# Kernel optimization log

Hardware: AMD Instinct MI355X
Metric: run time of the kernel (lower is better)

The kernel has to match this reference:

```python
import jax, jax.numpy as jnp
import numpy as np

B, H, W = 8, 512, 512          # batch, detector grid
M_PER_B = 32768
N = B * M_PER_B
C_IN, C_OUT, RED = 64, 128, 4
EPS = 1e-5


def setup_inputs() -> dict:
    key = jax.random.key(0)
    ks = jax.random.split(key, 8)
    # unique active-site indices per batch (permutation of flat grid cells)
    rng = np.random.default_rng(0)
    rows = []
    for b in range(B):
        flat = rng.permutation(H * W)[:M_PER_B]
        y, x = flat // W, flat % W
        rows.append(np.stack([np.full(M_PER_B, b), y, x], axis=1))
    indices = jnp.asarray(np.concatenate(rows, 0), dtype=jnp.int32)  # [N,3]

    feats = jax.random.normal(ks[0], (N, C_IN), jnp.float32)
    s1 = 1.0 / np.sqrt(9 * C_IN)
    s2 = 1.0 / np.sqrt(9 * C_OUT)
    return {
        "feats": feats,
        "indices": indices,
        "bn1_g": jnp.ones((C_IN,), jnp.float32),
        "bn1_b": jnp.zeros((C_IN,), jnp.float32),
        "w1": jax.random.normal(ks[1], (9, C_IN, C_OUT), jnp.float32) * s1,
        "bn2_g": jnp.ones((C_OUT,), jnp.float32),
        "bn2_b": jnp.zeros((C_OUT,), jnp.float32),
        "w2": jax.random.normal(ks[2], (9, C_OUT, C_OUT), jnp.float32) * s2,
        "fc1_w": jax.random.normal(ks[3], (C_OUT // RED, C_OUT), jnp.float32) / np.sqrt(C_OUT),
        "fc1_b": jnp.zeros((C_OUT // RED,), jnp.float32),
        "fc2_w": jax.random.normal(ks[4], (C_OUT, C_OUT // RED), jnp.float32) / np.sqrt(C_OUT // RED),
        "fc2_b": jnp.zeros((C_OUT,), jnp.float32),
        "w_skip": jax.random.normal(ks[5], (C_IN, C_OUT), jnp.float32) / np.sqrt(C_IN),
    }


def build_rulebook(indices):
    """Neighbor point-ids for each 3x3 offset. Returns ids [N,9], mask [N,9]."""
    n = indices.shape[0]
    b, y, x = indices[:, 0], indices[:, 1], indices[:, 2]
    grid = jnp.full((B, H, W), -1, jnp.int32).at[b, y, x].set(
        jnp.arange(n, dtype=jnp.int32))
    ids, masks = [], []
    for dy in (-1, 0, 1):
        for dx in (-1, 0, 1):
            ny, nx = y + dy, x + dx
            inb = (ny >= 0) & (ny < H) & (nx >= 0) & (nx < W)
            nid = grid[b, jnp.clip(ny, 0, H - 1), jnp.clip(nx, 0, W - 1)]
            m = inb & (nid >= 0)
            ids.append(jnp.where(m, nid, 0))
            masks.append(m)
    return jnp.stack(ids, 1), jnp.stack(masks, 1)


def subm_conv(f, nbr_ids, nbr_mask, w):
    """Submanifold 3x3 conv: gather-GEMM-scatter over active sites."""
    out = jnp.zeros((f.shape[0], w.shape[2]), f.dtype)
    for k in range(w.shape[0]):  # fixed 9 kernel offsets
        g = jnp.where(nbr_mask[:, k:k + 1], f[nbr_ids[:, k]], 0.0)
        out = out + g @ w[k]
    return out


def batchnorm(x, g, b):
    m = jnp.mean(x, 0)
    v = jnp.var(x, 0)  # biased, matches torch BN training normalization
    return (x - m) * jax.lax.rsqrt(v + EPS) * g + b


def reference(feats, indices, bn1_g, bn1_b, w1, bn2_g, bn2_b, w2,
              fc1_w, fc1_b, fc2_w, fc2_b, w_skip):
    nbr_ids, nbr_mask = build_rulebook(indices)  # shared indice_key rulebook
    bidx = indices[:, 0]

    out = jax.nn.relu(batchnorm(feats, bn1_g, bn1_b))
    out = subm_conv(out, nbr_ids, nbr_mask, w1)
    out = jax.nn.relu(batchnorm(out, bn2_g, bn2_b))
    out = subm_conv(out, nbr_ids, nbr_mask, w2)

    # SE: scatter-mean pool per event, FC-ReLU-FC-Sigmoid, per-site rescale
    pooled = jax.ops.segment_sum(out, bidx, num_segments=B)
    counts = jax.ops.segment_sum(jnp.ones((out.shape[0], 1), out.dtype), bidx,
                                 num_segments=B)
    pooled = pooled / jnp.clip(counts, 1.0, None)
    se = jax.nn.sigmoid(jax.nn.relu(pooled @ fc1_w.T + fc1_b) @ fc2_w.T + fc2_b)
    out = out * se[bidx]

    identity = feats @ w_skip  # 1x1 subm conv skip (in_ch != out_ch)
    return out + identity
```

## Files before the change

kernel.cpp:

```cpp
#include <hip/hip_runtime.h>
#include <math.h>

#define NPTS 262144
#define BB 8
#define HH 512
#define WW 512
#define EPSV 1e-5f

typedef short short8v __attribute__((ext_vector_type(8)));
typedef short short4v __attribute__((ext_vector_type(4)));
typedef float float4v __attribute__((ext_vector_type(4)));
typedef unsigned short ushort;
typedef ushort ushort8v __attribute__((ext_vector_type(8)));

static __device__ __forceinline__ ushort f2bf(float f) {
  union { float f; unsigned u; } v;
  v.f = f;
  unsigned r = v.u + 0x7fffu + ((v.u >> 16) & 1u);
  return (ushort)(r >> 16);
}

static __device__ __forceinline__ float bf2f(ushort h) {
  union { unsigned u; float f; } v;
  v.u = ((unsigned)h) << 16;
  return v.f;
}


__global__ __launch_bounds__(256) void k_scatter(const int* __restrict__ idx,
                                                 int* __restrict__ grid) {
  int i = blockIdx.x * 256 + threadIdx.x;
  int b = idx[i * 3 + 0], y = idx[i * 3 + 1], x = idx[i * 3 + 2];
  grid[(b * HH + y) * WW + x] = i;
}

__global__ __launch_bounds__(256) void k_rulebook(const int* __restrict__ idx,
                                                  const int* __restrict__ grid,
                                                  int* __restrict__ nbrT) {
  int i = blockIdx.x * 256 + threadIdx.x;
  int b = idx[i * 3 + 0], y = idx[i * 3 + 1], x = idx[i * 3 + 2];
  int t = 0;
  #pragma unroll
  for (int dy = -1; dy <= 1; ++dy) {
    #pragma unroll
    for (int dx = -1; dx <= 1; ++dx) {
      int ny = y + dy, nx = x + dx;
      int v = -1;
      if (ny >= 0 && ny < HH && nx >= 0 && nx < WW)
        v = grid[(b * HH + ny) * WW + nx];
      nbrT[(size_t)t * NPTS + i] = v;
      ++t;
    }
  }
}


__global__ __launch_bounds__(256) void k_stats64(const float* __restrict__ x,
                                                 float* __restrict__ sum,
                                                 float* __restrict__ ssum) {
  __shared__ float red_s[4][64];
  __shared__ float red_q[4][64];
  const int tid = threadIdx.x;
  const int lane = tid & 63;
  const int wave = tid >> 6;
  const int c4 = lane & 15;
  const int rq = lane >> 4;
  long long base = (long long)blockIdx.x * 256;
  float s0 = 0.f, s1 = 0.f, s2 = 0.f, s3 = 0.f;
  float q0 = 0.f, q1 = 0.f, q2 = 0.f, q3 = 0.f;
  for (int r = wave * 4 + rq; r < 256; r += 16) {
    float4 v = *(const float4*)(x + (base + r) * 64 + c4 * 4);
    s0 += v.x; s1 += v.y; s2 += v.z; s3 += v.w;
    q0 += v.x * v.x; q1 += v.y * v.y; q2 += v.z * v.z; q3 += v.w * v.w;
  }
  s0 += __shfl_xor(s0, 16, 64); s0 += __shfl_xor(s0, 32, 64);
  s1 += __shfl_xor(s1, 16, 64); s1 += __shfl_xor(s1, 32, 64);
  s2 += __shfl_xor(s2, 16, 64); s2 += __shfl_xor(s2, 32, 64);
  s3 += __shfl_xor(s3, 16, 64); s3 += __shfl_xor(s3, 32, 64);
  q0 += __shfl_xor(q0, 16, 64); q0 += __shfl_xor(q0, 32, 64);
  q1 += __shfl_xor(q1, 16, 64); q1 += __shfl_xor(q1, 32, 64);
  q2 += __shfl_xor(q2, 16, 64); q2 += __shfl_xor(q2, 32, 64);
  q3 += __shfl_xor(q3, 16, 64); q3 += __shfl_xor(q3, 32, 64);
  if (rq == 0) {
    red_s[wave][c4 * 4 + 0] = s0; red_s[wave][c4 * 4 + 1] = s1;
    red_s[wave][c4 * 4 + 2] = s2; red_s[wave][c4 * 4 + 3] = s3;
    red_q[wave][c4 * 4 + 0] = q0; red_q[wave][c4 * 4 + 1] = q1;
    red_q[wave][c4 * 4 + 2] = q2; red_q[wave][c4 * 4 + 3] = q3;
  }
  __syncthreads();
  if (tid < 64) {
    float ts = red_s[0][tid] + red_s[1][tid] + red_s[2][tid] + red_s[3][tid];
    float tq = red_q[0][tid] + red_q[1][tid] + red_q[2][tid] + red_q[3][tid];
    atomicAdd(&sum[tid], ts);
    atomicAdd(&ssum[tid], tq);
  }
}

template <int CI>
__global__ void k_finalize(const float* __restrict__ sum, const float* __restrict__ ssum,
                           const float* __restrict__ gam, const float* __restrict__ bet,
                           float* __restrict__ sc, float* __restrict__ sh) {
  int c = threadIdx.x;
  if (c < CI) {
    float m = sum[c] * (1.f / NPTS);
    float v = ssum[c] * (1.f / NPTS) - m * m;
    float s = gam[c] * rsqrtf(v + EPSV);
    sc[c] = s;
    sh[c] = bet[c] - m * s;
  }
}


__global__ __launch_bounds__(256) void k_norm1(const float* __restrict__ x,
                                               const float* __restrict__ sc,
                                               const float* __restrict__ sh,
                                               ushort* __restrict__ y) {
  long long i = ((long long)blockIdx.x * 256 + threadIdx.x) * 8;
  int c = (int)(i & 63);
  float4 a = *(const float4*)(x + i);
  float4 b = *(const float4*)(x + i + 4);
  float4 s0 = *(const float4*)(sc + c);
  float4 s1 = *(const float4*)(sc + c + 4);
  float4 h0 = *(const float4*)(sh + c);
  float4 h1 = *(const float4*)(sh + c + 4);
  ushort8v o;
  o[0] = f2bf(fmaxf(a.x * s0.x + h0.x, 0.f));
  o[1] = f2bf(fmaxf(a.y * s0.y + h0.y, 0.f));
  o[2] = f2bf(fmaxf(a.z * s0.z + h0.z, 0.f));
  o[3] = f2bf(fmaxf(a.w * s0.w + h0.w, 0.f));
  o[4] = f2bf(fmaxf(b.x * s1.x + h1.x, 0.f));
  o[5] = f2bf(fmaxf(b.y * s1.y + h1.y, 0.f));
  o[6] = f2bf(fmaxf(b.z * s1.z + h1.z, 0.f));
  o[7] = f2bf(fmaxf(b.w * s1.w + h1.w, 0.f));
  *(ushort8v*)(y + i) = o;
}

__global__ __launch_bounds__(256) void k_norm2(ushort* __restrict__ x,
                                               const float* __restrict__ sc,
                                               const float* __restrict__ sh) {
  long long i = ((long long)blockIdx.x * 256 + threadIdx.x) * 8;
  int c = (int)(i & 127);
  ushort8v v = *(const ushort8v*)(x + i);
  float4 s0 = *(const float4*)(sc + c);
  float4 s1 = *(const float4*)(sc + c + 4);
  float4 h0 = *(const float4*)(sh + c);
  float4 h1 = *(const float4*)(sh + c + 4);
  ushort8v o;
  o[0] = f2bf(fmaxf(bf2f(v[0]) * s0.x + h0.x, 0.f));
  o[1] = f2bf(fmaxf(bf2f(v[1]) * s0.y + h0.y, 0.f));
  o[2] = f2bf(fmaxf(bf2f(v[2]) * s0.z + h0.z, 0.f));
  o[3] = f2bf(fmaxf(bf2f(v[3]) * s0.w + h0.w, 0.f));
  o[4] = f2bf(fmaxf(bf2f(v[4]) * s1.x + h1.x, 0.f));
  o[5] = f2bf(fmaxf(bf2f(v[5]) * s1.y + h1.y, 0.f));
  o[6] = f2bf(fmaxf(bf2f(v[6]) * s1.z + h1.z, 0.f));
  o[7] = f2bf(fmaxf(bf2f(v[7]) * s1.w + h1.w, 0.f));
  *(ushort8v*)(x + i) = o;
}


__global__ __launch_bounds__(256) void k_wprep(const float* __restrict__ w,
                                               ushort* __restrict__ wt,
                                               int taps, int ci) {
  int i = blockIdx.x * 256 + threadIdx.x;
  int total = taps * ci * 128;
  if (i < total) {
    int t = i / (ci * 128);
    int rem = i - t * ci * 128;
    int c = rem >> 7;
    int o = rem & 127;
    wt[((size_t)t * 128 + o) * ci + c] = f2bf(w[i]);
  }
}


template <int CI, typename DstT, int EPI>
__global__ __launch_bounds__(256) void k_convd(const ushort* __restrict__ src,
                                               const int* __restrict__ nbrT,
                                               const ushort* __restrict__ wt,
                                               DstT* __restrict__ dst,
                                               float* __restrict__ e0,
                                               float* __restrict__ e1) {
  const int tid = threadIdx.x;
  const int base = blockIdx.x * 128;
  const int lane = tid & 63;
  const int wave = tid >> 6;
  const int wm = wave & 1, wn = wave >> 1;
  const int m_base = wm * 64, n_base = wn * 64;
  const int fm = lane & 15;
  const int fq = lane >> 4;
  const int koff = fq * 8;

  float4v acc[4][4];
  #pragma unroll
  for (int i = 0; i < 4; ++i)
    #pragma unroll
    for (int j = 0; j < 4; ++j) acc[i][j] = (float4v){0.f, 0.f, 0.f, 0.f};

  const int* nrow = nbrT + base + m_base + fm;

  for (int k = 0; k < 9; ++k) {
    int nid0 = nrow[(size_t)k * NPTS + 0];
    int nid1 = nrow[(size_t)k * NPTS + 16];
    int nid2 = nrow[(size_t)k * NPTS + 32];
    int nid3 = nrow[(size_t)k * NPTS + 48];
    const ushort* wrow = wt + ((size_t)k * 128 + n_base + fm) * CI + koff;
    #pragma unroll
    for (int kc = 0; kc < CI / 32; ++kc) {
      short8v bfr[4];
      #pragma unroll
      for (int ni = 0; ni < 4; ++ni)
        bfr[ni] = *(const short8v*)(wrow + ni * 16 * CI + kc * 32);
      const short8v z = {0, 0, 0, 0, 0, 0, 0, 0};
      short8v a0 = (nid0 >= 0) ? *(const short8v*)(src + (size_t)nid0 * CI + kc * 32 + koff) : z;
      short8v a1 = (nid1 >= 0) ? *(const short8v*)(src + (size_t)nid1 * CI + kc * 32 + koff) : z;
      short8v a2 = (nid2 >= 0) ? *(const short8v*)(src + (size_t)nid2 * CI + kc * 32 + koff) : z;
      short8v a3 = (nid3 >= 0) ? *(const short8v*)(src + (size_t)nid3 * CI + kc * 32 + koff) : z;
      #pragma unroll
      for (int ni = 0; ni < 4; ++ni) acc[0][ni] = __builtin_amdgcn_mfma_f32_16x16x32_bf16(a0, bfr[ni], acc[0][ni], 0, 0, 0);
      #pragma unroll
      for (int ni = 0; ni < 4; ++ni) acc[1][ni] = __builtin_amdgcn_mfma_f32_16x16x32_bf16(a1, bfr[ni], acc[1][ni], 0, 0, 0);
      #pragma unroll
      for (int ni = 0; ni < 4; ++ni) acc[2][ni] = __builtin_amdgcn_mfma_f32_16x16x32_bf16(a2, bfr[ni], acc[2][ni], 0, 0, 0);
      #pragma unroll
      for (int ni = 0; ni < 4; ++ni) acc[3][ni] = __builtin_amdgcn_mfma_f32_16x16x32_bf16(a3, bfr[ni], acc[3][ni], 0, 0, 0);
    }
  }

  float es[4], ess[4];
  if constexpr (EPI) {
    #pragma unroll
    for (int ni = 0; ni < 4; ++ni) { es[ni] = 0.f; ess[ni] = 0.f; }
  }
  #pragma unroll
  for (int mi = 0; mi < 4; ++mi) {
    #pragma unroll
    for (int ni = 0; ni < 4; ++ni) {
      int pt = base + m_base + mi * 16 + fq * 4;
      int co = n_base + ni * 16 + fm;
      float4v c = acc[mi][ni];
      #pragma unroll
      for (int r = 0; r < 4; ++r) {
        if constexpr (sizeof(DstT) == 4) {
          ((float*)dst)[(size_t)(pt + r) * 128 + co] = c[r];
          if constexpr (EPI == 2) es[ni] += c[r];
        } else {
          ushort h = f2bf(c[r]);
          ((ushort*)dst)[(size_t)(pt + r) * 128 + co] = h;
          if constexpr (EPI == 1) {
            float v = bf2f(h);
            es[ni] += v;
            ess[ni] += v * v;
          }
        }
      }
    }
  }

  if constexpr (EPI) {
    #pragma unroll
    for (int ni = 0; ni < 4; ++ni) {
      float s = es[ni];
      s += __shfl_xor(s, 16, 64);
      s += __shfl_xor(s, 32, 64);
      float q = 0.f;
      if constexpr (EPI == 1) {
        q = ess[ni];
        q += __shfl_xor(q, 16, 64);
        q += __shfl_xor(q, 32, 64);
      }
      if (fq == 0) {
        int co = n_base + ni * 16 + fm;
        if constexpr (EPI == 1) {
          atomicAdd(&e0[co], s);
          atomicAdd(&e1[co], q);
        } else {
          int b = base >> 15;
          atomicAdd(&e0[b * 128 + co], s);
        }
      }
    }
  }
}


template <typename SrcT, typename DstT, int CI, int TAPS, bool ACT, int EPI>
__global__ __launch_bounds__(256) void k_conv(const SrcT* __restrict__ src,
                                              const float* __restrict__ scale,
                                              const float* __restrict__ shift,
                                              const int* __restrict__ nbrT,
                                              const ushort* __restrict__ wt,
                                              DstT* __restrict__ dst,
                                              float* __restrict__ e0,
                                              float* __restrict__ e1) {
  constexpr int SA = CI + 8;
  __shared__ ushort As[128 * SA];
  __shared__ ushort Bs[128 * SA];
  __shared__ float s_sc[CI], s_sh[CI];

  const int tid = threadIdx.x;
  const int base = blockIdx.x * 128;
  const int lane = tid & 63;
  const int wave = tid >> 6;
  const int wm = wave & 1, wn = wave >> 1;
  const int m_base = wm * 64, n_base = wn * 64;
  const int fm = lane & 15;
  const int fq = lane >> 4;

  if constexpr (ACT) {
    for (int c = tid; c < CI; c += 256) {
      s_sc[c] = scale[c];
      s_sh[c] = shift[c];
    }
  }
  __syncthreads();

  float4v acc[4][4];
  #pragma unroll
  for (int i = 0; i < 4; ++i)
    #pragma unroll
    for (int j = 0; j < 4; ++j) acc[i][j] = (float4v){0.f, 0.f, 0.f, 0.f};

  const int srow_i = tid >> 1;
  const int shalf = tid & 1;
  const int c0 = shalf * (CI / 2);

  for (int k = 0; k < TAPS; ++k) {
    if (k) __syncthreads();

    int nid;
    if constexpr (TAPS == 1) {
      nid = base + srow_i;
    } else {
      nid = nbrT[(size_t)k * NPTS + base + srow_i];
    }
    ushort* arow = &As[srow_i * SA + c0];
    if (nid >= 0) {
      const SrcT* gsrc = src + (size_t)nid * CI + c0;
      if constexpr (sizeof(SrcT) == 4) {
        #pragma unroll
        for (int j = 0; j < CI / 2; j += 4) {
          float4 v = *(const float4*)((const float*)gsrc + j);
          if constexpr (ACT) {
            int c = c0 + j;
            v.x = fmaxf(v.x * s_sc[c + 0] + s_sh[c + 0], 0.f);
            v.y = fmaxf(v.y * s_sc[c + 1] + s_sh[c + 1], 0.f);
            v.z = fmaxf(v.z * s_sc[c + 2] + s_sh[c + 2], 0.f);
            v.w = fmaxf(v.w * s_sc[c + 3] + s_sh[c + 3], 0.f);
          }
          short4v o = {(short)f2bf(v.x), (short)f2bf(v.y), (short)f2bf(v.z), (short)f2bf(v.w)};
          *(short4v*)(arow + j) = o;
        }
      } else {
        #pragma unroll
        for (int j = 0; j < CI / 2; j += 8) {
          ushort8v raw = *(const ushort8v*)((const ushort*)gsrc + j);
          short8v o;
          #pragma unroll
          for (int e = 0; e < 8; ++e) {
            float f = bf2f(raw[e]);
            if constexpr (ACT) {
              int c = c0 + j + e;
              f = fmaxf(f * s_sc[c] + s_sh[c], 0.f);
            }
            o[e] = (short)f2bf(f);
          }
          *(short8v*)(arow + j) = o;
        }
      }
    } else {
      #pragma unroll
      for (int j = 0; j < CI / 2; j += 4)
        *(short4v*)(arow + j) = (short4v){0, 0, 0, 0};
    }

    {
      const ushort* wrow = wt + ((size_t)k * 128 + srow_i) * CI + c0;
      ushort* brow = &Bs[srow_i * SA + c0];
      #pragma unroll
      for (int j = 0; j < CI / 2; j += 8)
        *(uint4*)(brow + j) = *(const uint4*)(wrow + j);
    }
    __syncthreads();

    #pragma unroll
    for (int kc = 0; kc < CI / 32; ++kc) {
      short8v af[4], bf[4];
      #pragma unroll
      for (int mi = 0; mi < 4; ++mi)
        af[mi] = *(const short8v*)(&As[(m_base + mi * 16 + fm) * SA + kc * 32 + fq * 8]);
      #pragma unroll
      for (int ni = 0; ni < 4; ++ni)
        bf[ni] = *(const short8v*)(&Bs[(n_base + ni * 16 + fm) * SA + kc * 32 + fq * 8]);
      #pragma unroll
      for (int mi = 0; mi < 4; ++mi)
        #pragma unroll
        for (int ni = 0; ni < 4; ++ni)
          acc[mi][ni] = __builtin_amdgcn_mfma_f32_16x16x32_bf16(af[mi], bf[ni], acc[mi][ni], 0, 0, 0);
    }
  }

  float es[4], ess[4];
  if constexpr (EPI) {
    #pragma unroll
    for (int ni = 0; ni < 4; ++ni) { es[ni] = 0.f; ess[ni] = 0.f; }
  }
  #pragma unroll
  for (int mi = 0; mi < 4; ++mi) {
    #pragma unroll
    for (int ni = 0; ni < 4; ++ni) {
      int pt = base + m_base + mi * 16 + fq * 4;
      int co = n_base + ni * 16 + fm;
      float4v c = acc[mi][ni];
      #pragma unroll
      for (int r = 0; r < 4; ++r) {
        if constexpr (sizeof(DstT) == 4) {
          ((float*)dst)[(size_t)(pt + r) * 128 + co] = c[r];
          if constexpr (EPI == 2) es[ni] += c[r];
        } else {
          ushort h = f2bf(c[r]);
          ((ushort*)dst)[(size_t)(pt + r) * 128 + co] = h;
          if constexpr (EPI == 1) {
            float v = bf2f(h);
            es[ni] += v;
            ess[ni] += v * v;
          }
        }
      }
    }
  }

  if constexpr (EPI) {
    #pragma unroll
    for (int ni = 0; ni < 4; ++ni) {
      float s = es[ni];
      s += __shfl_xor(s, 16, 64);
      s += __shfl_xor(s, 32, 64);
      float q = 0.f;
      if constexpr (EPI == 1) {
        q = ess[ni];
        q += __shfl_xor(q, 16, 64);
        q += __shfl_xor(q, 32, 64);
      }
      if (fq == 0) {
        int co = n_base + ni * 16 + fm;
        if constexpr (EPI == 1) {
          atomicAdd(&e0[co], s);
          atomicAdd(&e1[co], q);
        } else {
          int b = base >> 15;
          atomicAdd(&e0[b * 128 + co], s);
        }
      }
    }
  }
}


__global__ __launch_bounds__(256) void k_se(const float* __restrict__ pooled,
                                            const float* __restrict__ fc1w,
                                            const float* __restrict__ fc1b,
                                            const float* __restrict__ fc2w,
                                            const float* __restrict__ fc2b,
                                            float* __restrict__ se) {
  __shared__ float h[8][32];
  int tid = threadIdx.x;
  int b = tid >> 5, j = tid & 31;
  float s = fc1b[j];
  for (int c = 0; c < 128; ++c)
    s += pooled[b * 128 + c] * (1.f / 32768.f) * fc1w[j * 128 + c];
  h[b][j] = fmaxf(s, 0.f);
  __syncthreads();
  for (int t = tid; t < 1024; t += 256) {
    int bb = t >> 7, c = t & 127;
    float s2 = fc2b[c];
    #pragma unroll
    for (int jj = 0; jj < 32; ++jj) s2 += h[bb][jj] * fc2w[c * 32 + jj];
    se[t] = 1.f / (1.f + expf(-s2));
  }
}

__global__ __launch_bounds__(256) void k_final(float* __restrict__ out,
                                               const ushort* __restrict__ id,
                                               const float* __restrict__ se) {
  long long i = ((long long)blockIdx.x * 256 + threadIdx.x) * 4;
  int co = (int)(i & 127);
  long long rowi = i >> 7;
  int b = (int)(rowi >> 15);
  float4 o = *(const float4*)(out + i);
  ushort dh[4];
  *(uint2*)dh = *(const uint2*)(id + i);
  float4 s = *(const float4*)(se + b * 128 + co);
  o.x = o.x * s.x + bf2f(dh[0]);
  o.y = o.y * s.y + bf2f(dh[1]);
  o.z = o.z * s.z + bf2f(dh[2]);
  o.w = o.w * s.w + bf2f(dh[3]);
  *(float4*)(out + i) = o;
}


extern "C" void kernel_launch(void* const* d_in, const int* in_sizes, int n_in,
                              void* d_out, int out_size, void* d_ws, size_t ws_size,
                              hipStream_t stream) {
  const float* feats = (const float*)d_in[0];
  const int* indices = (const int*)d_in[1];
  const float* bn1_g = (const float*)d_in[2];
  const float* bn1_b = (const float*)d_in[3];
  const float* w1    = (const float*)d_in[4];
  const float* bn2_g = (const float*)d_in[5];
  const float* bn2_b = (const float*)d_in[6];
  const float* w2    = (const float*)d_in[7];
  const float* fc1w  = (const float*)d_in[8];
  const float* fc1b  = (const float*)d_in[9];
  const float* fc2w  = (const float*)d_in[10];
  const float* fc2b  = (const float*)d_in[11];
  const float* wskip = (const float*)d_in[12];
  float* out = (float*)d_out;

  char* p = (char*)d_ws;
  int* nbrT = (int*)p;      p += (size_t)NPTS * 9 * 4;
  float* stats = (float*)p; p += 4096 * 4;
  ushort* wt1 = (ushort*)p; p += (size_t)9 * 128 * 64 * 2;
  ushort* wt2 = (ushort*)p; p += (size_t)9 * 128 * 128 * 2;
  ushort* wts = (ushort*)p; p += (size_t)128 * 64 * 2;
  p = (char*)(((size_t)p + 255) & ~(size_t)255);

  float* sum1 = stats, *ss1 = stats + 64, *sc1 = stats + 128, *sh1 = stats + 192;
  float* sum2 = stats + 256, *ss2 = stats + 384, *sc2 = stats + 512, *sh2 = stats + 640;
  float* pooled = stats + 768;
  float* se = stats + 1792;

  size_t fixed = (size_t)(p - (char*)d_ws);
  size_t need_new = fixed + (size_t)NPTS * 64 * 2 + (size_t)NPTS * 128 * 2;
  bool big = ws_size >= need_new;

  hipMemsetAsync(stats, 0, 4096 * 4, stream);

  if (big) {
    int* grid_i = (int*)p;
    ushort* featsn = (ushort*)p;
    ushort* out1 = (ushort*)(p + (size_t)NPTS * 64 * 2);

    hipMemsetAsync(grid_i, 0xFF, (size_t)BB * HH * WW * 4, stream);
    k_scatter<<<NPTS / 256, 256, 0, stream>>>(indices, grid_i);
    k_rulebook<<<NPTS / 256, 256, 0, stream>>>(indices, grid_i, nbrT);

    k_wprep<<<(9 * 64 * 128 + 255) / 256, 256, 0, stream>>>(w1, wt1, 9, 64);
    k_wprep<<<(9 * 128 * 128 + 255) / 256, 256, 0, stream>>>(w2, wt2, 9, 128);
    k_wprep<<<(64 * 128 + 255) / 256, 256, 0, stream>>>(wskip, wts, 1, 64);

    k_stats64<<<NPTS / 256, 256, 0, stream>>>(feats, sum1, ss1);
    k_finalize<64><<<1, 64, 0, stream>>>(sum1, ss1, bn1_g, bn1_b, sc1, sh1);

    k_norm1<<<NPTS * 64 / 8 / 256, 256, 0, stream>>>(feats, sc1, sh1, featsn);

    k_convd<64, ushort, 1><<<NPTS / 128, 256, 0, stream>>>(
        featsn, nbrT, wt1, out1, sum2, ss2);

    k_finalize<128><<<1, 128, 0, stream>>>(sum2, ss2, bn2_g, bn2_b, sc2, sh2);

    k_norm2<<<NPTS * 128 / 8 / 256, 256, 0, stream>>>(out1, sc2, sh2);

    k_convd<128, float, 2><<<NPTS / 128, 256, 0, stream>>>(
        out1, nbrT, wt2, out, pooled, nullptr);

    k_conv<float, ushort, 64, 1, false, 0><<<NPTS / 128, 256, 0, stream>>>(
        feats, nullptr, nullptr, nullptr, wts, out1, nullptr, nullptr);

    k_se<<<1, 256, 0, stream>>>(pooled, fc1w, fc1b, fc2w, fc2b, se);
    k_final<<<NPTS * 128 / 1024, 256, 0, stream>>>(out, out1, se);
  } else {
    int* grid_i = (int*)p;
    ushort* out1 = (ushort*)p;

    hipMemsetAsync(grid_i, 0xFF, (size_t)BB * HH * WW * 4, stream);
    k_scatter<<<NPTS / 256, 256, 0, stream>>>(indices, grid_i);
    k_rulebook<<<NPTS / 256, 256, 0, stream>>>(indices, grid_i, nbrT);

    k_wprep<<<(9 * 64 * 128 + 255) / 256, 256, 0, stream>>>(w1, wt1, 9, 64);
    k_wprep<<<(9 * 128 * 128 + 255) / 256, 256, 0, stream>>>(w2, wt2, 9, 128);
    k_wprep<<<(64 * 128 + 255) / 256, 256, 0, stream>>>(wskip, wts, 1, 64);

    k_stats64<<<NPTS / 256, 256, 0, stream>>>(feats, sum1, ss1);
    k_finalize<64><<<1, 64, 0, stream>>>(sum1, ss1, bn1_g, bn1_b, sc1, sh1);

    k_conv<float, ushort, 64, 9, true, 1><<<NPTS / 128, 256, 0, stream>>>(
        feats, sc1, sh1, nbrT, wt1, out1, sum2, ss2);

    k_finalize<128><<<1, 128, 0, stream>>>(sum2, ss2, bn2_g, bn2_b, sc2, sh2);

    k_conv<ushort, float, 128, 9, true, 2><<<NPTS / 128, 256, 0, stream>>>(
        out1, sc2, sh2, nbrT, wt2, out, pooled, nullptr);

    k_conv<float, ushort, 64, 1, false, 0><<<NPTS / 128, 256, 0, stream>>>(
        feats, nullptr, nullptr, nullptr, wts, out1, nullptr, nullptr);

    k_se<<<1, 256, 0, stream>>>(pooled, fc1w, fc1b, fc2w, fc2b, se);
    k_final<<<NPTS * 128 / 1024, 256, 0, stream>>>(out, out1, se);
  }
}
```

Measured before the change: 710.0 us.

## Stage gathered neighbor rows in swizzled LDS with register prefetch of next tap

The direct-gather conv kernel now gathers each tap's 128 neighbor feature rows cooperatively into XOR-swizzled shared memory. While MFMAs run on the current tap, it prefetches the next tap's gathered rows and the neighbor ids two taps ahead in registers. Previously each wave read the A fragments straight from global memory with 16-byte loads per lane. The block index is also remapped to interleave blocks across the point range. The change costs extra LDS, two barriers per tap, and more register pressure, which may reduce occupancy.

New measurement: 689.1 us. -2.9%, faster.

```diff
diff --git a/kernel.cpp b/kernel.cpp
--- a/kernel.cpp
+++ b/kernel.cpp
@@ -174,21 +174,31 @@
 
 
 template <int CI, typename DstT, int EPI>
-__global__ __launch_bounds__(256) void k_convd(const ushort* __restrict__ src,
+__global__ __launch_bounds__(256) void k_convp(const ushort* __restrict__ src,
                                                const int* __restrict__ nbrT,
                                                const ushort* __restrict__ wt,
                                                DstT* __restrict__ dst,
                                                float* __restrict__ e0,
                                                float* __restrict__ e1) {
+  constexpr int CHUNKS = CI / 8;
+  constexpr int RPI    = 64 / CHUNKS;
+  constexpr int NSTG   = 32 / RPI;
+  __shared__ ushort As[128 * CI];
+
   const int tid = threadIdx.x;
-  const int base = blockIdx.x * 128;
+  int bidx = blockIdx.x;
+  bidx = (bidx & 7) * ((NPTS / 128) / 8) + (bidx >> 3);
+  const int base = bidx * 128;
   const int lane = tid & 63;
   const int wave = tid >> 6;
   const int wm = wave & 1, wn = wave >> 1;
   const int m_base = wm * 64, n_base = wn * 64;
   const int fm = lane & 15;
   const int fq = lane >> 4;
-  const int koff = fq * 8;
+
+  const int s_rl = lane / CHUNKS;
+  const int s_c  = lane % CHUNKS;
+  const int srow0 = wave * 32 + s_rl;
 
   float4v acc[4][4];
   #pragma unroll
@@ -196,33 +206,74 @@
     #pragma unroll
     for (int j = 0; j < 4; ++j) acc[i][j] = (float4v){0.f, 0.f, 0.f, 0.f};
 
-  const int* nrow = nbrT + base + m_base + fm;
-
+  int nr[2][NSTG];
+  uint4 g[NSTG];
+
+  #pragma unroll
+  for (int i = 0; i < NSTG; ++i)
+    nr[0][i] = nbrT[base + srow0 + i * RPI];
+  #pragma unroll
+  for (int i = 0; i < NSTG; ++i)
+    nr[1][i] = nbrT[(size_t)NPTS + base + srow0 + i * RPI];
+
+  #pragma unroll
+  for (int i = 0; i < NSTG; ++i) {
+    int nid = nr[0][i];
+    uint4 gv = {0u, 0u, 0u, 0u};
+    if (nid >= 0) gv = *(const uint4*)(src + (size_t)nid * CI + s_c * 8);
+    g[i] = gv;
+  }
+  #pragma unroll
+  for (int i = 0; i < NSTG; ++i) {
+    int row = srow0 + i * RPI;
+    *(uint4*)(&As[row * CI + ((s_c ^ (row & 7)) << 3)]) = g[i];
+  }
+  __syncthreads();
+
+  #pragma unroll
   for (int k = 0; k < 9; ++k) {
-    int nid0 = nrow[(size_t)k * NPTS + 0];
-    int nid1 = nrow[(size_t)k * NPTS + 16];
-    int nid2 = nrow[(size_t)k * NPTS + 32];
-    int nid3 = nrow[(size_t)k * NPTS + 48];
-    const ushort* wrow = wt + ((size_t)k * 128 + n_base + fm) * CI + koff;
+    if (k < 8) {
+      #pragma unroll
+      for (int i = 0; i < NSTG; ++i) {
+        int nid = nr[(k + 1) & 1][i];
+        uint4 gv = {0u, 0u, 0u, 0u};
+        if (nid >= 0) gv = *(const uint4*)(src + (size_t)nid * CI + s_c * 8);
+        g[i] = gv;
+      }
+    }
+    if (k < 7) {
+      #pragma unroll
+      for (int i = 0; i < NSTG; ++i)
+        nr[k & 1][i] = nbrT[(size_t)(k + 2) * NPTS + base + srow0 + i * RPI];
+    }
+
+    const ushort* wrow = wt + ((size_t)k * 128 + n_base + fm) * CI + fq * 8;
     #pragma unroll
     for (int kc = 0; kc < CI / 32; ++kc) {
-      short8v bfr[4];
+      short8v af[4], bfr[4];
+      #pragma unroll
+      for (int mi = 0; mi < 4; ++mi) {
+        int R = m_base + mi * 16 + fm;
+        af[mi] = *(const short8v*)(&As[R * CI + (((kc * 4 + fq) ^ (fm & 7)) << 3)]);
+      }
       #pragma unroll
       for (int ni = 0; ni < 4; ++ni)
         bfr[ni] = *(const short8v*)(wrow + ni * 16 * CI + kc * 32);
-      const short8v z = {0, 0, 0, 0, 0, 0, 0, 0};
-      short8v a0 = (nid0 >= 0) ? *(const short8v*)(src + (size_t)nid0 * CI + kc * 32 + koff) : z;
-      short8v a1 = (nid1 >= 0) ? *(const short8v*)(src + (size_t)nid1 * CI + kc * 32 + koff) : z;
-      short8v a2 = (nid2 >= 0) ? *(const short8v*)(src + (size_t)nid2 * CI + kc * 32 + koff) : z;
-      short8v a3 = (nid3 >= 0) ? *(const short8v*)(src + (size_t)nid3 * CI + kc * 32 + koff) : z;
-      #pragma unroll
-      for (int ni = 0; ni < 4; ++ni) acc[0][ni] = __builtin_amdgcn_mfma_f32_16x16x32_bf16(a0, bfr[ni], acc[0][ni], 0, 0, 0);
-      #pragma unroll
-      for (int ni = 0; ni < 4; ++ni) acc[1][ni] = __builtin_amdgcn_mfma_f32_16x16x32_bf16(a1, bfr[ni], acc[1][ni], 0, 0, 0);
-      #pragma unroll
-      for (int ni = 0; ni < 4; ++ni) acc[2][ni] = __builtin_amdgcn_mfma_f32_16x16x32_bf16(a2, bfr[ni], acc[2][ni], 0, 0, 0);
-      #pragma unroll
-      for (int ni = 0; ni < 4; ++ni) acc[3][ni] = __builtin_amdgcn_mfma_f32_16x16x32_bf16(a3, bfr[ni], acc[3][ni], 0, 0, 0);
+      #pragma unroll
+      for (int mi = 0; mi < 4; ++mi)
+        #pragma unroll
+        for (int ni = 0; ni < 4; ++ni)
+          acc[mi][ni] = __builtin_amdgcn_mfma_f32_16x16x32_bf16(af[mi], bfr[ni], acc[mi][ni], 0, 0, 0);
+    }
+
+    if (k < 8) {
+      __syncthreads();
+      #pragma unroll
+      for (int i = 0; i < NSTG; ++i) {
+        int row = srow0 + i * RPI;
+        *(uint4*)(&As[row * CI + ((s_c ^ (row & 7)) << 3)]) = g[i];
+      }
+      __syncthreads();
     }
   }
 
@@ -553,14 +604,14 @@
 
     k_norm1<<<NPTS * 64 / 8 / 256, 256, 0, stream>>>(feats, sc1, sh1, featsn);
 
-    k_convd<64, ushort, 1><<<NPTS / 128, 256, 0, stream>>>(
+    k_convp<64, ushort, 1><<<NPTS / 128, 256, 0, stream>>>(
         featsn, nbrT, wt1, out1, sum2, ss2);
 
     k_finalize<128><<<1, 128, 0, stream>>>(sum2, ss2, bn2_g, bn2_b, sc2, sh2);
 
     k_norm2<<<NPTS * 128 / 8 / 256, 256, 0, stream>>>(out1, sc2, sh2);
 
-    k_convd<128, float, 2><<<NPTS / 128, 256, 0, stream>>>(
+    k_convp<128, float, 2><<<NPTS / 128, 256, 0, stream>>>(
         out1, nbrT, wt2, out, pooled, nullptr);
 
     k_conv<float, ushort, 64, 1, false, 0><<<NPTS / 128, 256, 0, stream>>>(
```
